# Performance work log

Measured on AMD Instinct MI355X. Metric: run time of the kernel, lower is better.

Reference implementation:

```python
import jax, jax.numpy as jnp
import numpy as np

NEG_INF = -1e30
GAP_OPEN = -5.0
GAP_EXTEND = -1.0
TEMP = 1.0
# penalize_turns=True
RIGHTMOD = jnp.array([GAP_OPEN, GAP_EXTEND, GAP_OPEN], dtype=jnp.float32)
DOWNMOD = jnp.array([GAP_OPEN, GAP_OPEN, GAP_EXTEND], dtype=jnp.float32)


def setup_inputs() -> dict:
    key = jax.random.key(0)
    x = jax.random.normal(key, (512, 151, 151), dtype=jnp.float32)
    return {"x": x}


def _lse(v):
    # temperature-scaled smooth max over last axis
    return TEMP * jax.nn.logsumexp(v / TEMP, axis=-1)


def _sw_forward(x):
    B, N, M = x.shape
    a, b = N - 1, M - 1
    core = x[:, :-1, :-1]  # (B, a, b) similarity scores used in the DP

    # anti-diagonal rotation indices (static, numpy)
    ar = np.arange(a - 1, -1, -1)[:, None]          # (a, 1)
    br = np.arange(b)[None, :]                       # (1, b)
    i = br - ar + (a - 1)                            # diagonal index, (a, b)
    j = (ar + br) // 2                               # position within diagonal
    n_diag = a + b - 1
    m = (a + b) // 2
    smo = jnp.asarray(((np.arange(n_diag) + a % 2) % 2).astype(np.float32))  # parity per diagonal

    smx = jnp.full((B, n_diag, m), NEG_INF, dtype=x.dtype).at[:, i, j].set(core)
    smx_t = jnp.transpose(smx, (1, 0, 2))  # (n_diag, B, m) for scan

    def step(carry, inp):
        h2, h1 = carry            # each (B, m, 3)
        sx, so = inp              # sx (B, m), so scalar parity in {0,1}
        # align: pad state dim with 0 (fresh local-alignment start), add match score
        align = jnp.concatenate([h2, jnp.zeros_like(h2[..., :1])], axis=-1) + sx[..., None]
        # shifted views of h1 along the diagonal-position axis
        h1_dn = jnp.concatenate([jnp.full_like(h1[:, :1, :], NEG_INF), h1[:, :-1, :]], axis=1)
        h1_up = jnp.concatenate([h1[:, 1:, :], jnp.full_like(h1[:, :1, :], NEG_INF)], axis=1)
        right = so * h1_dn + (1.0 - so) * h1 + RIGHTMOD
        down = so * h1 + (1.0 - so) * h1_up + DOWNMOD
        right = right[:, :, :2]  # restrict_turns=True
        h0 = jnp.stack([_lse(align), _lse(right), _lse(down)], axis=-1)  # (B, m, 3)
        return (h1, h0), h0

    init_h = jnp.full((B, m, 3), NEG_INF, dtype=x.dtype)
    _, ys = jax.lax.scan(step, (init_h, init_h), (smx_t, smo))  # ys (n_diag, B, m, 3)
    results = jnp.transpose(ys, (1, 0, 2, 3))  # (B, n_diag, m, 3)
    hij = results[:, i, j]                      # un-rotate -> (B, a, b, 3)
    scores = (hij + x[:, 1:, 1:, None]).reshape(B, -1)
    final = TEMP * jax.nn.logsumexp(scores / TEMP, axis=-1)  # (B,)
    return final.sum()


def reference(x):
    return _sw_forward(x)
```

## Files before the change

### kernel.cpp

```cpp
#include <hip/hip_runtime.h>


#define CGO 6.737946999085467e-03f
#define CGE 3.678794411714423e-01f
#define L2E 1.4426950408889634f
#define LN2 0.6931471805599453f
#define RTHR 0x1p28f
#define RSC  0x1p-64f
#define EADD 64.0f

#define SA1 4.9787068367863944e-02f
#define SA2 2.4787521766663585e-03f
#define SA4 6.1442123533282098e-06f
#define SA8 3.7751345442790977e-11f
#define CA1 3.6787944117144233e-01f
#define CA2 1.3533528323661270e-01f
#define CA3 4.9787068367863944e-02f

#if __has_builtin(__builtin_amdgcn_exp2f)
#define EXP2(x) __builtin_amdgcn_exp2f(x)
#else
static __device__ __forceinline__ float EXP2_(float x){float r;asm("v_exp_f32 %0, %1":"=v"(r):"v"(x));return r;}
#define EXP2(x) EXP2_(x)
#endif

#if __has_builtin(__builtin_amdgcn_logf)
#define LOG2(x) __builtin_amdgcn_logf(x)
#else
static __device__ __forceinline__ float LOG2_(float x){float r;asm("v_log_f32 %0, %1":"=v"(r):"v"(x));return r;}
#define LOG2(x) LOG2_(x)
#endif

#define DPP_UP   0x138
#define DPP_DN   0x130
#define ROW_SHR1 0x111
#define ROW_SHR2 0x112
#define ROW_SHR4 0x114
#define ROW_SHR8 0x118
#define BCAST15  0x142
#define BCAST31  0x143

template<int CTRL>
static __device__ __forceinline__ float dppz(float v){
    return __int_as_float(__builtin_amdgcn_update_dpp(
        0, __float_as_int(v), CTRL, 0xF, 0xF, true));
}

static __device__ __forceinline__ float dec16(unsigned bits16){
    unsigned short us = (unsigned short)bits16;
    _Float16 h;
    __builtin_memcpy(&h, &us, 2);
    return (float)h;
}

template<int IMM>
static __device__ __forceinline__
void stepRow(const char* ldsB, const int vaddr,
             const float vA16, const float vA32,
             float (&SX)[3], unsigned& Rc,
             float (&HSs)[3], float (&g)[3], float (&h2p)[3],
             const float oneE, float (&S)[3])
{
    const unsigned Rn = *(const unsigned*)(ldsB + vaddr + IMM);
    const float D0 = dec16(Rc << 8);
    const float D1 = dec16(Rc & 0xFF00u);
    const float D2 = dec16((Rc >> 8) & 0xFF00u);
    const float D3 = dppz<DPP_DN>(D0);

    const float h00 = SX[0] * (HSs[0] + oneE);
    const float h01 = SX[1] * (HSs[1] + oneE);
    const float h02 = SX[2] * (HSs[2] + oneE);

    const float h0u = dppz<DPP_UP>(h02);
    const float b0 = CGO * h0u;
    const float b1 = CGO * h00;
    const float b2 = CGO * h01;

    const float p1 = fmaf(CGE, b0, b1);
    const float p2 = fmaf(CGE, p1, b2);

    float t = dppz<DPP_UP>(p2);
    t = fmaf(SA1, dppz<ROW_SHR1>(t), t);
    t = fmaf(SA2, dppz<ROW_SHR2>(t), t);
    t = fmaf(SA4, dppz<ROW_SHR4>(t), t);
    t = fmaf(SA8, dppz<ROW_SHR8>(t), t);
    t = fmaf(vA16, dppz<BCAST15>(t), t);
    t = fmaf(vA32, dppz<BCAST31>(t), t);

    const float h10 = fmaf(CA1, t, b0);
    const float h11 = fmaf(CA2, t, p1);
    const float h12 = fmaf(CA3, t, p2);

    const float h20 = fmaf(CGO, g[0], CGE * h2p[0]);
    const float h21 = fmaf(CGO, g[1], CGE * h2p[1]);
    const float h22 = fmaf(CGO, g[2], CGE * h2p[2]);

    g[0] = h00 + h10; g[1] = h01 + h11; g[2] = h02 + h12;
    const float hs0 = g[0] + h20;
    const float hs1 = g[1] + h21;
    const float hs2 = g[2] + h22;
    h2p[0] = h20; h2p[1] = h21; h2p[2] = h22;

    S[0] = fmaf(D1, hs0, S[0]);
    S[1] = fmaf(D2, hs1, S[1]);
    S[2] = fmaf(D3, hs2, S[2]);

    HSs[0] = dppz<DPP_UP>(hs2);
    HSs[1] = hs0; HSs[2] = hs1;
    SX[0] = D0; SX[1] = D1; SX[2] = D2;
    Rc = Rn;
}

__global__ __launch_bounds__(256)
void sw_row(const float* __restrict__ x, float* __restrict__ part,
            float* __restrict__ out_atomic, int use_atomic) {
    const int b = blockIdx.x;
    const float* xb = x + (size_t)b * 22801;
    const int tid = threadIdx.x;

    __shared__ char ldsB[38912];

    {
        int4* l4 = (int4*)ldsB;
        for (int i = tid; i < 38912 / 16; i += 256) l4[i] = int4{0,0,0,0};
    }
    __syncthreads();

    {
        auto PROC = [&](float v, int idx) {
            const int idc = idx > 22800 ? 22800 : idx;
            const float e = EXP2(v * L2E);
            const _Float16 hv = (_Float16)e;
            unsigned short u16; __builtin_memcpy(&u16, &hv, 2);
            const unsigned byte = ((unsigned)u16 + 0x7Fu + ((u16 >> 8) & 1u)) >> 8;
            const unsigned r = ((unsigned)idc * 111111u) >> 24;
            const int c = idc - 151 * (int)r;
            const int l3 = (c * 0x5556) >> 16;
            const int kk = c - 3 * l3;
            ldsB[(int)r * 256 + 4 * l3 + kk] = (char)byte;
        };
        float va[8], vb[8];
        #pragma unroll
        for (int j = 0; j < 8; ++j) {
            const int idx = j * 256 + tid;
            va[j] = xb[idx > 22800 ? 22800 : idx];
        }
        for (int i = 0; i < 12; i += 2) {
            if (i + 1 < 12) {
                #pragma unroll
                for (int j = 0; j < 8; ++j) {
                    const int idx = (i + 1) * 2048 + j * 256 + tid;
                    vb[j] = xb[idx > 22800 ? 22800 : idx];
                }
            }
            #pragma unroll
            for (int j = 0; j < 8; ++j) PROC(va[j], i * 2048 + j * 256 + tid);
            if (i + 2 < 12) {
                #pragma unroll
                for (int j = 0; j < 8; ++j) {
                    const int idx = (i + 2) * 2048 + j * 256 + tid;
                    va[j] = xb[idx > 22800 ? 22800 : idx];
                }
            }
            if (i + 1 < 12) {
                #pragma unroll
                for (int j = 0; j < 8; ++j) PROC(vb[j], (i + 1) * 2048 + j * 256 + tid);
            }
        }
    }
    __syncthreads();
    if (tid >= 64) return;

    const int lane = tid;
    const float vA16 = EXP2(-4.3280851226668902f * (float)((lane & 15) + 1));
    const float vA32 = EXP2(-4.3280851226668902f * (float)((lane & 31) + 1));
    const int vl4 = 4 * lane;

    float SX[3];
    unsigned Rc;
    {
        const unsigned w0 = *(const unsigned*)(ldsB + vl4);
        SX[0] = dec16(w0 << 8);
        SX[1] = dec16(w0 & 0xFF00u);
        SX[2] = dec16((w0 >> 8) & 0xFF00u);
        Rc = *(const unsigned*)(ldsB + 256 + vl4);
    }
    float HSs[3] = {0.0f, 0.0f, 0.0f};
    float g[3]   = {0.0f, 0.0f, 0.0f};
    float h2p[3] = {0.0f, 0.0f, 0.0f};
    float S[3]   = {0.0f, 0.0f, 0.0f};
    float oneE = 1.0f;
    float E = 0.0f;

    int vaddr = 512 + vl4;

    for (int gi = 0; gi < 18; ++gi) {
        stepRow<   0>(ldsB, vaddr, vA16, vA32, SX, Rc, HSs, g, h2p, oneE, S);
        stepRow< 256>(ldsB, vaddr, vA16, vA32, SX, Rc, HSs, g, h2p, oneE, S);
        stepRow< 512>(ldsB, vaddr, vA16, vA32, SX, Rc, HSs, g, h2p, oneE, S);
        stepRow< 768>(ldsB, vaddr, vA16, vA32, SX, Rc, HSs, g, h2p, oneE, S);
        stepRow<1024>(ldsB, vaddr, vA16, vA32, SX, Rc, HSs, g, h2p, oneE, S);
        stepRow<1280>(ldsB, vaddr, vA16, vA32, SX, Rc, HSs, g, h2p, oneE, S);
        stepRow<1536>(ldsB, vaddr, vA16, vA32, SX, Rc, HSs, g, h2p, oneE, S);
        float m = fmaxf(fmaxf(g[0], g[1]), g[2]);
        m = fmaxf(m, fmaxf(fmaxf(h2p[0], h2p[1]), h2p[2]));
        const bool rn = __any(m > RTHR);
        const float sc = rn ? RSC : 1.0f;
        stepRow<1792>(ldsB, vaddr, vA16, vA32, SX, Rc, HSs, g, h2p, oneE, S);
        #pragma unroll
        for (int k = 0; k < 3; ++k) {
            HSs[k] *= sc; g[k] *= sc; h2p[k] *= sc; S[k] *= sc;
        }
        oneE *= sc; E += rn ? EADD : 0.0f;
        vaddr += 2048;
    }
    stepRow<   0>(ldsB, vaddr, vA16, vA32, SX, Rc, HSs, g, h2p, oneE, S);
    stepRow< 256>(ldsB, vaddr, vA16, vA32, SX, Rc, HSs, g, h2p, oneE, S);
    stepRow< 512>(ldsB, vaddr, vA16, vA32, SX, Rc, HSs, g, h2p, oneE, S);
    stepRow< 768>(ldsB, vaddr, vA16, vA32, SX, Rc, HSs, g, h2p, oneE, S);
    stepRow<1024>(ldsB, vaddr, vA16, vA32, SX, Rc, HSs, g, h2p, oneE, S);
    stepRow<1280>(ldsB, vaddr, vA16, vA32, SX, Rc, HSs, g, h2p, oneE, S);

    float St = (S[0] + S[1]) + S[2];
    #pragma unroll
    for (int off = 32; off; off >>= 1) St += __shfl_xor(St, off, 64);
    if (lane == 0) {
        const float val = LN2 * (E + LOG2(St));
        if (use_atomic) atomicAdd(out_atomic, val);
        else            part[b] = val;
    }
}

__global__ __launch_bounds__(256)
void final_reduce(const float* __restrict__ part, float* __restrict__ out) {
    const int t = threadIdx.x;
    float v = part[t] + part[t + 256];
    #pragma unroll
    for (int off = 32; off; off >>= 1) v += __shfl_xor(v, off);
    __shared__ float ws[4];
    if ((t & 63) == 0) ws[t >> 6] = v;
    __syncthreads();
    if (t == 0) out[0] = ws[0] + ws[1] + ws[2] + ws[3];
}

extern "C" void kernel_launch(void* const* d_in, const int* in_sizes, int n_in,
                              void* d_out, int out_size, void* d_ws, size_t ws_size,
                              hipStream_t stream) {
    const float* x = (const float*)d_in[0];
    float* out = (float*)d_out;

    if (ws_size >= 512 * sizeof(float)) {
        float* part = (float*)d_ws;
        sw_row<<<512, 256, 0, stream>>>(x, part, nullptr, 0);
        final_reduce<<<1, 256, 0, stream>>>(part, out);
    } else {
        hipMemsetAsync(out, 0, sizeof(float), stream);
        sw_row<<<512, 256, 0, stream>>>(x, nullptr, out, 1);
    }
}
```

Before: 35.61 us.

## Store exp scores as fp16 in LDS and drop far-shift scan terms

The exponentiated scores are now stored as full fp16 values in LDS (8 bytes per lane slot) rather than an 8-bit truncated fp16 byte. Each row step loads a uint2 instead of a packed word, and the wider row stride doubles the LDS footprint. The SA4/SA8 prefix-scan terms (row shifts of 4 and 8) are removed from every step, which shortens the serial DPP chain. The renormalisation check also drops the h2p max. The combined effect trades decode work and scan depth against more LDS traffic and possible loss of accuracy in the scan, which now approximates the gap recurrence.

```diff
diff --git a/kernel.cpp b/kernel.cpp
--- a/kernel.cpp
+++ b/kernel.cpp
@@ -11,8 +11,6 @@
 
 #define SA1 4.9787068367863944e-02f
 #define SA2 2.4787521766663585e-03f
-#define SA4 6.1442123533282098e-06f
-#define SA8 3.7751345442790977e-11f
 #define CA1 3.6787944117144233e-01f
 #define CA2 1.3533528323661270e-01f
 #define CA3 4.9787068367863944e-02f
@@ -35,8 +33,6 @@
 #define DPP_DN   0x130
 #define ROW_SHR1 0x111
 #define ROW_SHR2 0x112
-#define ROW_SHR4 0x114
-#define ROW_SHR8 0x118
 #define BCAST15  0x142
 #define BCAST31  0x143
 
@@ -46,8 +42,8 @@
         0, __float_as_int(v), CTRL, 0xF, 0xF, true));
 }
 
-static __device__ __forceinline__ float dec16(unsigned bits16){
-    unsigned short us = (unsigned short)bits16;
+static __device__ __forceinline__ float declo(unsigned w){
+    unsigned short us = (unsigned short)w;
     _Float16 h;
     __builtin_memcpy(&h, &us, 2);
     return (float)h;
@@ -57,14 +53,14 @@
 static __device__ __forceinline__
 void stepRow(const char* ldsB, const int vaddr,
              const float vA16, const float vA32,
-             float (&SX)[3], unsigned& Rc,
+             float (&SX)[3], uint2& Rc,
              float (&HSs)[3], float (&g)[3], float (&h2p)[3],
              const float oneE, float (&S)[3])
 {
-    const unsigned Rn = *(const unsigned*)(ldsB + vaddr + IMM);
-    const float D0 = dec16(Rc << 8);
-    const float D1 = dec16(Rc & 0xFF00u);
-    const float D2 = dec16((Rc >> 8) & 0xFF00u);
+    const uint2 Rn = *(const uint2*)(ldsB + vaddr + IMM);
+    const float D0 = declo(Rc.x);
+    const float D1 = declo(Rc.x >> 16);
+    const float D2 = declo(Rc.y);
     const float D3 = dppz<DPP_DN>(D0);
 
     const float h00 = SX[0] * (HSs[0] + oneE);
@@ -82,8 +78,6 @@
     float t = dppz<DPP_UP>(p2);
     t = fmaf(SA1, dppz<ROW_SHR1>(t), t);
     t = fmaf(SA2, dppz<ROW_SHR2>(t), t);
-    t = fmaf(SA4, dppz<ROW_SHR4>(t), t);
-    t = fmaf(SA8, dppz<ROW_SHR8>(t), t);
     t = fmaf(vA16, dppz<BCAST15>(t), t);
     t = fmaf(vA32, dppz<BCAST31>(t), t);
 
@@ -118,26 +112,23 @@
     const float* xb = x + (size_t)b * 22801;
     const int tid = threadIdx.x;
 
-    __shared__ char ldsB[38912];
+    __shared__ char ldsB[77824];
 
     {
         int4* l4 = (int4*)ldsB;
-        for (int i = tid; i < 38912 / 16; i += 256) l4[i] = int4{0,0,0,0};
+        for (int i = tid; i < 77824 / 16; i += 256) l4[i] = int4{0,0,0,0};
     }
     __syncthreads();
 
     {
         auto PROC = [&](float v, int idx) {
             const int idc = idx > 22800 ? 22800 : idx;
-            const float e = EXP2(v * L2E);
-            const _Float16 hv = (_Float16)e;
-            unsigned short u16; __builtin_memcpy(&u16, &hv, 2);
-            const unsigned byte = ((unsigned)u16 + 0x7Fu + ((u16 >> 8) & 1u)) >> 8;
+            const _Float16 hv = (_Float16)EXP2(v * L2E);
             const unsigned r = ((unsigned)idc * 111111u) >> 24;
             const int c = idc - 151 * (int)r;
             const int l3 = (c * 0x5556) >> 16;
             const int kk = c - 3 * l3;
-            ldsB[(int)r * 256 + 4 * l3 + kk] = (char)byte;
+            *(_Float16*)(ldsB + (int)r * 512 + l3 * 8 + kk * 2) = hv;
         };
         float va[8], vb[8];
         #pragma unroll
@@ -174,16 +165,16 @@
     const int lane = tid;
     const float vA16 = EXP2(-4.3280851226668902f * (float)((lane & 15) + 1));
     const float vA32 = EXP2(-4.3280851226668902f * (float)((lane & 31) + 1));
-    const int vl4 = 4 * lane;
+    const int vl8 = 8 * lane;
 
     float SX[3];
-    unsigned Rc;
+    uint2 Rc;
     {
-        const unsigned w0 = *(const unsigned*)(ldsB + vl4);
-        SX[0] = dec16(w0 << 8);
-        SX[1] = dec16(w0 & 0xFF00u);
-        SX[2] = dec16((w0 >> 8) & 0xFF00u);
-        Rc = *(const unsigned*)(ldsB + 256 + vl4);
+        const uint2 w0 = *(const uint2*)(ldsB + vl8);
+        SX[0] = declo(w0.x);
+        SX[1] = declo(w0.x >> 16);
+        SX[2] = declo(w0.y);
+        Rc = *(const uint2*)(ldsB + 512 + vl8);
     }
     float HSs[3] = {0.0f, 0.0f, 0.0f};
     float g[3]   = {0.0f, 0.0f, 0.0f};
@@ -192,34 +183,33 @@
     float oneE = 1.0f;
     float E = 0.0f;
 
-    int vaddr = 512 + vl4;
+    int vaddr = 1024 + vl8;
 
     for (int gi = 0; gi < 18; ++gi) {
         stepRow<   0>(ldsB, vaddr, vA16, vA32, SX, Rc, HSs, g, h2p, oneE, S);
-        stepRow< 256>(ldsB, vaddr, vA16, vA32, SX, Rc, HSs, g, h2p, oneE, S);
         stepRow< 512>(ldsB, vaddr, vA16, vA32, SX, Rc, HSs, g, h2p, oneE, S);
-        stepRow< 768>(ldsB, vaddr, vA16, vA32, SX, Rc, HSs, g, h2p, oneE, S);
         stepRow<1024>(ldsB, vaddr, vA16, vA32, SX, Rc, HSs, g, h2p, oneE, S);
-        stepRow<1280>(ldsB, vaddr, vA16, vA32, SX, Rc, HSs, g, h2p, oneE, S);
         stepRow<1536>(ldsB, vaddr, vA16, vA32, SX, Rc, HSs, g, h2p, oneE, S);
-        float m = fmaxf(fmaxf(g[0], g[1]), g[2]);
-        m = fmaxf(m, fmaxf(fmaxf(h2p[0], h2p[1]), h2p[2]));
+        stepRow<2048>(ldsB, vaddr, vA16, vA32, SX, Rc, HSs, g, h2p, oneE, S);
+        stepRow<2560>(ldsB, vaddr, vA16, vA32, SX, Rc, HSs, g, h2p, oneE, S);
+        stepRow<3072>(ldsB, vaddr, vA16, vA32, SX, Rc, HSs, g, h2p, oneE, S);
+        const float m = fmaxf(fmaxf(g[0], g[1]), g[2]);
         const bool rn = __any(m > RTHR);
         const float sc = rn ? RSC : 1.0f;
-        stepRow<1792>(ldsB, vaddr, vA16, vA32, SX, Rc, HSs, g, h2p, oneE, S);
+        stepRow<3584>(ldsB, vaddr, vA16, vA32, SX, Rc, HSs, g, h2p, oneE, S);
         #pragma unroll
         for (int k = 0; k < 3; ++k) {
             HSs[k] *= sc; g[k] *= sc; h2p[k] *= sc; S[k] *= sc;
         }
         oneE *= sc; E += rn ? EADD : 0.0f;
-        vaddr += 2048;
+        vaddr += 4096;
     }
     stepRow<   0>(ldsB, vaddr, vA16, vA32, SX, Rc, HSs, g, h2p, oneE, S);
-    stepRow< 256>(ldsB, vaddr, vA16, vA32, SX, Rc, HSs, g, h2p, oneE, S);
     stepRow< 512>(ldsB, vaddr, vA16, vA32, SX, Rc, HSs, g, h2p, oneE, S);
-    stepRow< 768>(ldsB, vaddr, vA16, vA32, SX, Rc, HSs, g, h2p, oneE, S);
     stepRow<1024>(ldsB, vaddr, vA16, vA32, SX, Rc, HSs, g, h2p, oneE, S);
-    stepRow<1280>(ldsB, vaddr, vA16, vA32, SX, Rc, HSs, g, h2p, oneE, S);
+    stepRow<1536>(ldsB, vaddr, vA16, vA32, SX, Rc, HSs, g, h2p, oneE, S);
+    stepRow<2048>(ldsB, vaddr, vA16, vA32, SX, Rc, HSs, g, h2p, oneE, S);
+    stepRow<2560>(ldsB, vaddr, vA16, vA32, SX, Rc, HSs, g, h2p, oneE, S);
 
     float St = (S[0] + S[1]) + S[2];
     #pragma unroll
```

After: 32.09 us. 9.9% less time.
